# Performance work log

Measured on AMD Instinct MI355X. Metric: run time of the kernel, lower is better.

The kernel has to match this reference:

```python
import jax, jax.numpy as jnp
import numpy as np

B, T, I, H, NM = 128, 512, 2, 1024, 8
MS = H // NM  # module size = 128


def setup_inputs() -> dict:
    key = jax.random.key(0)
    ks = jax.random.split(key, 6)
    s = 1.0 / np.sqrt(H)
    return {
        "x": jax.random.normal(ks[0], (B, T + 1, I, 1), jnp.float32),
        "W_ih": jax.random.normal(ks[1], (H, I), jnp.float32) * s,
        "W_hh": jax.random.normal(ks[2], (H, H), jnp.float32) * s,
        "fc_w": jax.random.normal(ks[3], (I, H), jnp.float32) * s,
        "fc_b": jax.random.normal(ks[4], (I,), jnp.float32) * s,
        "enc_w": jax.random.normal(ks[5], (H, I), jnp.float32) * s,
    }


def reference(x, W_ih, W_hh, fc_w, fc_b, enc_w):
    # x: [B, T+1, I, 1] -> squeeze trailing dim
    xs = x[..., 0]                       # [B, T+1, I]
    h0 = xs[:, 0] @ enc_w.T              # start_encoder (no bias) -> [B, H]

    # Clockwork block structure: row-module i reads hidden cols >= i*MS.
    mod_idx = jnp.arange(H) // MS
    mask_hh = (mod_idx[None, :] >= mod_idx[:, None]).astype(W_hh.dtype)
    Whh_m = W_hh * mask_hh               # block upper-triangular recurrent weights
    periods = 2 ** jnp.arange(NM)        # module clock periods [1,2,4,...,128]

    def step(h, inp):
        x_t, t = inp                     # x_t: [B, I], t: scalar step index
        cand = jnp.tanh(x_t @ W_ih.T + h @ Whh_m.T)          # [B, H]
        active = jnp.repeat((t % periods) == 0, MS)          # [H] unit-level clock mask
        h_new = jnp.where(active[None, :], cand, h)          # inactive modules keep state
        return h_new, h_new @ fc_w.T + fc_b                  # fc output per step

    _, outs = jax.lax.scan(step, h0, (jnp.swapaxes(xs[:, 1:], 0, 1), jnp.arange(T)))
    return jnp.swapaxes(outs, 0, 1)      # [B, T, I]
```

## Files before the change

### kernel.cpp

```cpp
#include <hip/hip_runtime.h>
#include <hip/hip_fp16.h>
#include <math.h>

#define Bsz 128
#define Tsz 512
#define Hsz 1024
#define MS  128
#define NT  512


__global__ __launch_bounds__(256)
void retile_whh(const float* __restrict__ W, __half* __restrict__ WBr) {
    const int p = blockIdx.x + 1;
    const int t = threadIdx.x;
    int c = 0;
    while ((c+1)*(c+2)/2 <= p) ++c;
    const int r = p - c*(c+1)/2;
    __half* wb = WBr + (size_t)(p-1) * MS * MS;
    for (int o = t; o < MS*MS; o += 256) {
        const int k  = o >> 12;
        const int tt = (o >> 3) & 511;
        const int e  = o & 7;
        const int row = tt >> 2, jq = tt & 3;
        const int col = jq*32 + (((k + jq) & 3) << 3) + e;
        wb[o] = __float2half(W[(size_t)(r*MS+row)*Hsz + c*MS + col]);
    }
}

__device__ __forceinline__ float fast_tanh(float x) {
    const float e = __expf(2.0f * x);
    return 1.0f - 2.0f * __builtin_amdgcn_rcpf(e + 1.0f);
}

template <int CTRL>
__device__ __forceinline__ float dpp_get(float v) {
    union { float f; int i; } u, o;
    u.f = v;
    o.i = __builtin_amdgcn_update_dpp(0, u.i, CTRL, 0xf, 0xf, true);
    return o.f;
}

__device__ __forceinline__ void pk_fma(float2& acc, float2 a, float2 b) {
    asm("v_pk_fma_f32 %0, %1, %2, %0" : "+v"(acc) : "v"(a), "v"(b));
}

union H4 { short4 s4; __half2 h2[2]; };
union F4 { float4 v; float2 h[2]; };

__global__ __launch_bounds__(NT)
void cwrnn_kernel(const float* __restrict__ x,
                  const float* __restrict__ W_ih,
                  const float* __restrict__ fc_w,
                  const float* __restrict__ fc_b,
                  const float* __restrict__ enc_w,
                  const float* __restrict__ Whh,
                  const __half* __restrict__ WBr,
                  float* __restrict__ out)
{
    __shared__ __half  WL[3*MS*MS];
    __shared__ float   Sp2s[36][MS];
    __shared__ float   h_s[Hsz];
    __shared__ float   H0[2][MS];
    __shared__ float2  x_s[Tsz+1];
    __shared__ float2  wih_s[Hsz];
    __shared__ float2  fcw_s[Hsz];
    __shared__ float2  OpM0[2][8];
    __shared__ float2  OpHi[16];
    __shared__ float2  OpHiN[16];

    const int tid   = threadIdx.x;
    const int lane  = tid & 63;
    const int wave  = tid >> 6;
    const int b     = blockIdx.x;
    const int row00 = tid >> 2;
    const int jc    = tid & 3;

    const float2* xb = (const float2*)(x + (size_t)b*(Tsz+1)*2);
    float* outb = out + (size_t)b*Tsz*2;

    for (int i = tid; i < Tsz+1; i += NT) x_s[i] = xb[i];
    for (int i = tid; i < Hsz; i += NT) wih_s[i] = ((const float2*)W_ih)[i];
    for (int i = tid; i < Hsz; i += NT) fcw_s[i] = make_float2(fc_w[i], fc_w[Hsz+i]);
    {
        const int PSEL[3] = {2, 4, 5};
        for (int i = tid; i < 3*MS*MS/8; i += NT) {
            const int pi = i >> 11, rem = i & 2047;
            ((int4*)WL)[i] =
                ((const int4*)(WBr + (size_t)(PSEL[pi]-1)*MS*MS))[rem];
        }
    }
    if (tid < 16) { OpHi[tid] = make_float2(0.f,0.f); OpHiN[tid] = make_float2(0.f,0.f); }
    const float fb0 = fc_b[0], fb1 = fc_b[1];

    F4 w00[8];
    #pragma unroll
    for (int u = 0; u < 8; ++u) {
        const int uu = (u + 2*jc) & 7;
        w00[u].v = *(const float4*)(Whh + (size_t)row00*Hsz + jc*32 + uu*4);
    }
    short4 w01[8], w02[8];
    #pragma unroll
    for (int k = 0; k < 4; ++k) {
        *(int4*)(&w01[2*k]) = *(const int4*)(WBr + (size_t)0*MS*MS + k*4096 + tid*8);
        *(int4*)(&w02[2*k]) = *(const int4*)(WBr + (size_t)2*MS*MS + k*4096 + tid*8);
    }

    {
        const float2 x0 = xb[0];
        for (int i = tid; i < Hsz; i += NT) {
            const float2 ew = ((const float2*)enc_w)[i];
            const float v = x0.x*ew.x + x0.y*ew.y;
            h_s[i] = v;
            if (i < MS) H0[0][i] = v;
        }
    }
    __syncthreads();

    float R1=0.f,R2=0.f,R3=0.f,R4=0.f,R5=0.f,R6=0.f,R7=0.f;

    auto load_hq = [&](int c, F4* hq) {
        #pragma unroll
        for (int u = 0; u < 8; ++u) {
            const int uu = (u + 2*jc) & 7;
            hq[u].v = *(const float4*)(h_s + c*MS + jc*32 + uu*4);
        }
    };
    auto pair_acc16 = [&](const short4* w, const F4* hq) -> float {
        float2 a0 = {0.f,0.f}, a1 = {0.f,0.f};
        #pragma unroll
        for (int u = 0; u < 8; ++u) {
            H4 ww; ww.s4 = w[u];
            pk_fma(a0, __half22float2(ww.h2[0]), hq[u].h[0]);
            pk_fma(a1, __half22float2(ww.h2[1]), hq[u].h[1]);
        }
        return (a0.x + a0.y) + (a1.x + a1.y);
    };
    auto wl_read = [&](int pi, short4* w) {
        const __half* base = WL + (size_t)pi*MS*MS + tid*8;
        #pragma unroll
        for (int k = 0; k < 4; ++k)
            *(int4*)(&w[2*k]) = *(const int4*)(base + k*4096);
    };
    auto wg_load = [&](int p, short4* w) {
        const __half* base = WBr + (size_t)(p-1)*MS*MS + tid*8;
        #pragma unroll
        for (int k = 0; k < 4; ++k)
            *(int4*)(&w[2*k]) = *(const int4*)(base + k*4096);
    };

    auto do_cols = [&](int ashad) {
        F4 hq[8];
        short4 wA[8], wB[8];
        if (ashad >= 3) wg_load(6, wA);
        load_hq(1, hq);
        wl_read(0, wB);
        R1 = pair_acc16(w01, hq);
        { float aa = pair_acc16(wB, hq);
          aa += dpp_get<0xB1>(aa); aa += dpp_get<0x4E>(aa);
          if (jc == 0) Sp2s[2][row00] = aa; }
        if (ashad >= 2) {
            load_hq(2, hq);
            R2 = pair_acc16(w02, hq);
            wl_read(1, wB);
            { float aa = pair_acc16(wB, hq);
              aa += dpp_get<0xB1>(aa); aa += dpp_get<0x4E>(aa);
              if (jc == 0) Sp2s[4][row00] = aa; }
            wl_read(2, wB);
            { float aa = pair_acc16(wB, hq);
              aa += dpp_get<0xB1>(aa); aa += dpp_get<0x4E>(aa);
              if (jc == 0) Sp2s[5][row00] = aa; }
        }
        if (ashad >= 3) {
            load_hq(3, hq);
            int cc = 3, rr = 0;
            while (true) {
                int rn = rr + 1, cn = cc;
                if (rn > cn) { cn += 1; rn = 0; }
                const bool hn = (cn <= ashad);
                if (hn) wg_load(cn*(cn+1)/2 + rn, wB);
                float aa = pair_acc16(wA, hq);
                if (rr == 0) {
                    switch (cc) {
                        case 3: R3 = aa; break;
                        case 4: R4 = aa; break;
                        case 5: R5 = aa; break;
                        case 6: R6 = aa; break;
                        default: R7 = aa; break;
                    }
                } else {
                    aa += dpp_get<0xB1>(aa); aa += dpp_get<0x4E>(aa);
                    if (jc == 0) Sp2s[cc*(cc+1)/2 + rr][row00] = aa;
                }
                if (!hn) break;
                if (cn != cc) load_hq(cn, hq);
                cc = cn; rr = rn;
                #pragma unroll
                for (int u = 0; u < 8; ++u) wA[u] = wB[u];
            }
        }
    };

    do_cols(7);
    __syncthreads();

    for (int t = 0; t < Tsz; ++t) {
        const int A  = (t == 0) ? 7 : ((t & 1) ? 0 : min(__ffs(t)-1, 7));
        const int ap = (t & 1) ? ((t == 1) ? 7 : min(__ffs(t-1)-1, 7)) : 0;
        const float2 xt = x_s[t+1];

        if (ap >= 1) do_cols(ap);

        {
            const float* h0r = H0[t & 1];
            float2 a0 = {0.f,0.f}, a1 = {0.f,0.f};
            #pragma unroll
            for (int u = 0; u < 8; ++u) {
                const int uu = (u + 2*jc) & 7;
                F4 hv; hv.v = *(const float4*)(h0r + jc*32 + uu*4);
                pk_fma(a0, w00[u].h[0], hv.h[0]);
                pk_fma(a1, w00[u].h[1], hv.h[1]);
            }
            float a = (a0.x + a0.y) + (a1.x + a1.y);
            a += ((R1+R2)+(R3+R4)) + ((R5+R6)+R7);
            a += dpp_get<0xB1>(a); a += dpp_get<0x4E>(a);
            const float2 wih0 = wih_s[row00];
            const float hv0 = fast_tanh(a + xt.x*wih0.x + xt.y*wih0.y);
            if (jc == 0) H0[(t+1)&1][row00] = hv0;
            const float2 fw0 = fcw_s[row00];
            float o0 = (jc == 0) ? hv0*fw0.x : 0.f;
            float o1 = (jc == 0) ? hv0*fw0.y : 0.f;
            o0 += dpp_get<0x111>(o0); o1 += dpp_get<0x111>(o1);
            o0 += dpp_get<0x112>(o0); o1 += dpp_get<0x112>(o1);
            o0 += dpp_get<0x114>(o0); o1 += dpp_get<0x114>(o1);
            o0 += dpp_get<0x118>(o0); o1 += dpp_get<0x118>(o1);
            o0 += dpp_get<0x142>(o0); o1 += dpp_get<0x142>(o1);
            o0 += dpp_get<0x143>(o0); o1 += dpp_get<0x143>(o1);
            if (lane == 63) OpM0[t&1][wave] = make_float2(o0, o1);
        }

        if (A >= 1) {
            const int nrows = (A+1)*MS;
            {
                const int g = MS + tid;
                if (g < nrows) {
                    const int r = g >> 7, il = g & (MS-1);
                    float sc[8];
                    #pragma unroll
                    for (int c = 1; c < 8; ++c)
                        sc[c] = Sp2s[c*(c+1)/2 + ((c < r) ? c : r)][il];
                    const float2 wih2 = wih_s[g];
                    float pre = xt.x*wih2.x + xt.y*wih2.y;
                    #pragma unroll
                    for (int c = 1; c < 8; ++c) pre += (c >= r) ? sc[c] : 0.f;
                    const float hv = fast_tanh(pre);
                    h_s[g] = hv;
                    const float2 fw = fcw_s[g];
                    float o0 = hv*fw.x, o1 = hv*fw.y;
                    o0 += dpp_get<0x111>(o0); o1 += dpp_get<0x111>(o1);
                    o0 += dpp_get<0x112>(o0); o1 += dpp_get<0x112>(o1);
                    o0 += dpp_get<0x114>(o0); o1 += dpp_get<0x114>(o1);
                    o0 += dpp_get<0x118>(o0); o1 += dpp_get<0x118>(o1);
                    o0 += dpp_get<0x142>(o0); o1 += dpp_get<0x142>(o1);
                    o0 += dpp_get<0x143>(o0); o1 += dpp_get<0x143>(o1);
                    if (lane == 63) OpHiN[2 + wave] = make_float2(o0, o1);
                }
            }
            {
                const int g = 5*MS + tid;
                if (g < nrows) {
                    const int r = g >> 7, il = g & (MS-1);
                    float sc[8];
                    #pragma unroll
                    for (int c = 1; c < 8; ++c)
                        sc[c] = Sp2s[c*(c+1)/2 + ((c < r) ? c : r)][il];
                    const float2 wih2 = wih_s[g];
                    float pre = xt.x*wih2.x + xt.y*wih2.y;
                    #pragma unroll
                    for (int c = 1; c < 8; ++c) pre += (c >= r) ? sc[c] : 0.f;
                    const float hv = fast_tanh(pre);
                    h_s[g] = hv;
                    const float2 fw = fcw_s[g];
                    float o0 = hv*fw.x, o1 = hv*fw.y;
                    o0 += dpp_get<0x111>(o0); o1 += dpp_get<0x111>(o1);
                    o0 += dpp_get<0x112>(o0); o1 += dpp_get<0x112>(o1);
                    o0 += dpp_get<0x114>(o0); o1 += dpp_get<0x114>(o1);
                    o0 += dpp_get<0x118>(o0); o1 += dpp_get<0x118>(o1);
                    o0 += dpp_get<0x142>(o0); o1 += dpp_get<0x142>(o1);
                    o0 += dpp_get<0x143>(o0); o1 += dpp_get<0x143>(o1);
                    if (lane == 63) OpHiN[10 + wave] = make_float2(o0, o1);
                }
            }
        }

        if (t > 0 && tid == 0) {
            const int tp = t - 1;
            if (ap >= 1) {
                for (int k = 2; k <= 2*ap+1; ++k) OpHi[k] = OpHiN[k];
            }
            float o0 = fb0, o1 = fb1;
            #pragma unroll
            for (int w = 0; w < 8; ++w) { o0 += OpM0[tp&1][w].x; o1 += OpM0[tp&1][w].y; }
            #pragma unroll
            for (int k = 2; k < 16; ++k) { o0 += OpHi[k].x; o1 += OpHi[k].y; }
            *(float2*)(outb + 2*tp) = make_float2(o0, o1);
        }

        __syncthreads();
    }

    if (tid == 0) {
        float o0 = fb0, o1 = fb1;
        #pragma unroll
        for (int w = 0; w < 8; ++w) { o0 += OpM0[1][w].x; o1 += OpM0[1][w].y; }
        #pragma unroll
        for (int k = 2; k < 16; ++k) { o0 += OpHi[k].x; o1 += OpHi[k].y; }
        *(float2*)(outb + 2*(Tsz-1)) = make_float2(o0, o1);
    }
}

extern "C" void kernel_launch(void* const* d_in, const int* in_sizes, int n_in,
                              void* d_out, int out_size, void* d_ws, size_t ws_size,
                              hipStream_t stream) {
    const float* x     = (const float*)d_in[0];
    const float* W_ih  = (const float*)d_in[1];
    const float* W_hh  = (const float*)d_in[2];
    const float* fc_w  = (const float*)d_in[3];
    const float* fc_b  = (const float*)d_in[4];
    const float* enc_w = (const float*)d_in[5];
    float* outp = (float*)d_out;
    __half* WBr = (__half*)((char*)d_ws + 65536);

    retile_whh<<<35, 256, 0, stream>>>(W_hh, WBr);
    cwrnn_kernel<<<Bsz, NT, 0, stream>>>(x, W_ih, fc_w, fc_b, enc_w, W_hh, WBr, outp);
}
```

Baseline: 906.7 us.

## Double block threads to 1024 with 8 lanes per row and buffer outputs in LDS

Raises the per-batch workgroup from 512 to 1024 threads. Each hidden row is now split across 8 lanes instead of 4, so every thread holds half as many weights and h values, and the cross-lane reduction gains one extra DPP stage. The retile kernel's weight layout is changed to match the 8-lane split. The two per-thread row passes in the high-module update become a single pass, and the per-step output writes go into a shared buffer that is copied to global memory once at the end. The aim is to cut the per-thread serial FMA chain inside each latency-bound timestep. In exchange, each step's barriers now cover twice as many waves and the register budget per thread is tighter.

```diff
diff --git a/kernel.cpp b/kernel.cpp
--- a/kernel.cpp
+++ b/kernel.cpp
@@ -6,7 +6,7 @@
 #define Tsz 512
 #define Hsz 1024
 #define MS  128
-#define NT  512
+#define NT  1024
 
 
 __global__ __launch_bounds__(256)
@@ -18,11 +18,12 @@
     const int r = p - c*(c+1)/2;
     __half* wb = WBr + (size_t)(p-1) * MS * MS;
     for (int o = t; o < MS*MS; o += 256) {
-        const int k  = o >> 12;
-        const int tt = (o >> 3) & 511;
+        const int k  = o >> 13;
+        const int tt = (o >> 3) & 1023;
         const int e  = o & 7;
-        const int row = tt >> 2, jq = tt & 3;
-        const int col = jq*32 + (((k + jq) & 3) << 3) + e;
+        const int row = tt >> 3, jq = tt & 7;
+        const int chunk = ((2*k + (e >> 2)) + jq) & 3;
+        const int col = jq*16 + chunk*4 + (e & 3);
         wb[o] = __float2half(W[(size_t)(r*MS+row)*Hsz + c*MS + col]);
     }
 }
@@ -64,16 +65,16 @@
     __shared__ float2  x_s[Tsz+1];
     __shared__ float2  wih_s[Hsz];
     __shared__ float2  fcw_s[Hsz];
-    __shared__ float2  OpM0[2][8];
+    __shared__ float2  OpM0[2][16];
     __shared__ float2  OpHi[16];
     __shared__ float2  OpHiN[16];
+    __shared__ float   out_s[Tsz*2];
 
     const int tid   = threadIdx.x;
-    const int lane  = tid & 63;
     const int wave  = tid >> 6;
     const int b     = blockIdx.x;
-    const int row00 = tid >> 2;
-    const int jc    = tid & 3;
+    const int row00 = tid >> 3;
+    const int jc    = tid & 7;
 
     const float2* xb = (const float2*)(x + (size_t)b*(Tsz+1)*2);
     float* outb = out + (size_t)b*Tsz*2;
@@ -92,17 +93,17 @@
     if (tid < 16) { OpHi[tid] = make_float2(0.f,0.f); OpHiN[tid] = make_float2(0.f,0.f); }
     const float fb0 = fc_b[0], fb1 = fc_b[1];
 
-    F4 w00[8];
+    F4 w00[4];
     #pragma unroll
-    for (int u = 0; u < 8; ++u) {
-        const int uu = (u + 2*jc) & 7;
-        w00[u].v = *(const float4*)(Whh + (size_t)row00*Hsz + jc*32 + uu*4);
-    }
-    short4 w01[8], w02[8];
+    for (int u = 0; u < 4; ++u) {
+        const int uu = (u + jc) & 3;
+        w00[u].v = *(const float4*)(Whh + (size_t)row00*Hsz + jc*16 + uu*4);
+    }
+    short4 w01[4], w02[4];
     #pragma unroll
-    for (int k = 0; k < 4; ++k) {
-        *(int4*)(&w01[2*k]) = *(const int4*)(WBr + (size_t)0*MS*MS + k*4096 + tid*8);
-        *(int4*)(&w02[2*k]) = *(const int4*)(WBr + (size_t)2*MS*MS + k*4096 + tid*8);
+    for (int k = 0; k < 2; ++k) {
+        *(int4*)(&w01[2*k]) = *(const int4*)(WBr + (size_t)0*MS*MS + k*8192 + tid*8);
+        *(int4*)(&w02[2*k]) = *(const int4*)(WBr + (size_t)2*MS*MS + k*8192 + tid*8);
     }
 
     {
@@ -120,54 +121,57 @@
 
     auto load_hq = [&](int c, F4* hq) {
         #pragma unroll
-        for (int u = 0; u < 8; ++u) {
-            const int uu = (u + 2*jc) & 7;
-            hq[u].v = *(const float4*)(h_s + c*MS + jc*32 + uu*4);
+        for (int u = 0; u < 4; ++u) {
+            const int uu = (u + jc) & 3;
+            hq[u].v = *(const float4*)(h_s + c*MS + jc*16 + uu*4);
         }
     };
     auto pair_acc16 = [&](const short4* w, const F4* hq) -> float {
         float2 a0 = {0.f,0.f}, a1 = {0.f,0.f};
         #pragma unroll
-        for (int u = 0; u < 8; ++u) {
+        for (int u = 0; u < 4; ++u) {
             H4 ww; ww.s4 = w[u];
             pk_fma(a0, __half22float2(ww.h2[0]), hq[u].h[0]);
             pk_fma(a1, __half22float2(ww.h2[1]), hq[u].h[1]);
         }
         return (a0.x + a0.y) + (a1.x + a1.y);
     };
+    auto red8 = [&](float a) -> float {
+        a += dpp_get<0xB1>(a);
+        a += dpp_get<0x4E>(a);
+        a += dpp_get<0x141>(a);
+        return a;
+    };
     auto wl_read = [&](int pi, short4* w) {
         const __half* base = WL + (size_t)pi*MS*MS + tid*8;
         #pragma unroll
-        for (int k = 0; k < 4; ++k)
-            *(int4*)(&w[2*k]) = *(const int4*)(base + k*4096);
+        for (int k = 0; k < 2; ++k)
+            *(int4*)(&w[2*k]) = *(const int4*)(base + k*8192);
     };
     auto wg_load = [&](int p, short4* w) {
         const __half* base = WBr + (size_t)(p-1)*MS*MS + tid*8;
         #pragma unroll
-        for (int k = 0; k < 4; ++k)
-            *(int4*)(&w[2*k]) = *(const int4*)(base + k*4096);
+        for (int k = 0; k < 2; ++k)
+            *(int4*)(&w[2*k]) = *(const int4*)(base + k*8192);
     };
 
     auto do_cols = [&](int ashad) {
-        F4 hq[8];
-        short4 wA[8], wB[8];
+        F4 hq[4];
+        short4 wA[4], wB[4];
         if (ashad >= 3) wg_load(6, wA);
         load_hq(1, hq);
         wl_read(0, wB);
         R1 = pair_acc16(w01, hq);
-        { float aa = pair_acc16(wB, hq);
-          aa += dpp_get<0xB1>(aa); aa += dpp_get<0x4E>(aa);
+        { float aa = red8(pair_acc16(wB, hq));
           if (jc == 0) Sp2s[2][row00] = aa; }
         if (ashad >= 2) {
             load_hq(2, hq);
             R2 = pair_acc16(w02, hq);
             wl_read(1, wB);
-            { float aa = pair_acc16(wB, hq);
-              aa += dpp_get<0xB1>(aa); aa += dpp_get<0x4E>(aa);
+            { float aa = red8(pair_acc16(wB, hq));
               if (jc == 0) Sp2s[4][row00] = aa; }
             wl_read(2, wB);
-            { float aa = pair_acc16(wB, hq);
-              aa += dpp_get<0xB1>(aa); aa += dpp_get<0x4E>(aa);
+            { float aa = red8(pair_acc16(wB, hq));
               if (jc == 0) Sp2s[5][row00] = aa; }
         }
         if (ashad >= 3) {
@@ -188,14 +192,14 @@
                         default: R7 = aa; break;
                     }
                 } else {
-                    aa += dpp_get<0xB1>(aa); aa += dpp_get<0x4E>(aa);
+                    aa = red8(aa);
                     if (jc == 0) Sp2s[cc*(cc+1)/2 + rr][row00] = aa;
                 }
                 if (!hn) break;
                 if (cn != cc) load_hq(cn, hq);
                 cc = cn; rr = rn;
                 #pragma unroll
-                for (int u = 0; u < 8; ++u) wA[u] = wB[u];
+                for (int u = 0; u < 4; ++u) wA[u] = wB[u];
             }
         }
     };
@@ -214,15 +218,15 @@
             const float* h0r = H0[t & 1];
             float2 a0 = {0.f,0.f}, a1 = {0.f,0.f};
             #pragma unroll
-            for (int u = 0; u < 8; ++u) {
-                const int uu = (u + 2*jc) & 7;
-                F4 hv; hv.v = *(const float4*)(h0r + jc*32 + uu*4);
+            for (int u = 0; u < 4; ++u) {
+                const int uu = (u + jc) & 3;
+                F4 hv; hv.v = *(const float4*)(h0r + jc*16 + uu*4);
                 pk_fma(a0, w00[u].h[0], hv.h[0]);
                 pk_fma(a1, w00[u].h[1], hv.h[1]);
             }
             float a = (a0.x + a0.y) + (a1.x + a1.y);
             a += ((R1+R2)+(R3+R4)) + ((R5+R6)+R7);
-            a += dpp_get<0xB1>(a); a += dpp_get<0x4E>(a);
+            a = red8(a);
             const float2 wih0 = wih_s[row00];
             const float hv0 = fast_tanh(a + xt.x*wih0.x + xt.y*wih0.y);
             if (jc == 0) H0[(t+1)&1][row00] = hv0;
@@ -235,87 +239,64 @@
             o0 += dpp_get<0x118>(o0); o1 += dpp_get<0x118>(o1);
             o0 += dpp_get<0x142>(o0); o1 += dpp_get<0x142>(o1);
             o0 += dpp_get<0x143>(o0); o1 += dpp_get<0x143>(o1);
-            if (lane == 63) OpM0[t&1][wave] = make_float2(o0, o1);
+            if ((tid & 63) == 63) OpM0[t&1][wave] = make_float2(o0, o1);
         }
 
         if (A >= 1) {
             const int nrows = (A+1)*MS;
-            {
-                const int g = MS + tid;
-                if (g < nrows) {
-                    const int r = g >> 7, il = g & (MS-1);
-                    float sc[8];
-                    #pragma unroll
-                    for (int c = 1; c < 8; ++c)
-                        sc[c] = Sp2s[c*(c+1)/2 + ((c < r) ? c : r)][il];
-                    const float2 wih2 = wih_s[g];
-                    float pre = xt.x*wih2.x + xt.y*wih2.y;
-                    #pragma unroll
-                    for (int c = 1; c < 8; ++c) pre += (c >= r) ? sc[c] : 0.f;
-                    const float hv = fast_tanh(pre);
-                    h_s[g] = hv;
-                    const float2 fw = fcw_s[g];
-                    float o0 = hv*fw.x, o1 = hv*fw.y;
-                    o0 += dpp_get<0x111>(o0); o1 += dpp_get<0x111>(o1);
-                    o0 += dpp_get<0x112>(o0); o1 += dpp_get<0x112>(o1);
-                    o0 += dpp_get<0x114>(o0); o1 += dpp_get<0x114>(o1);
-                    o0 += dpp_get<0x118>(o0); o1 += dpp_get<0x118>(o1);
-                    o0 += dpp_get<0x142>(o0); o1 += dpp_get<0x142>(o1);
-                    o0 += dpp_get<0x143>(o0); o1 += dpp_get<0x143>(o1);
-                    if (lane == 63) OpHiN[2 + wave] = make_float2(o0, o1);
-                }
+            const int g = MS + tid;
+            if (g < nrows) {
+                const int r = g >> 7, il = g & (MS-1);
+                float sc[8];
+                #pragma unroll
+                for (int c = 1; c < 8; ++c)
+                    sc[c] = Sp2s[c*(c+1)/2 + ((c < r) ? c : r)][il];
+                const float2 wih2 = wih_s[g];
+                float pre = xt.x*wih2.x + xt.y*wih2.y;
+                #pragma unroll
+                for (int c = 1; c < 8; ++c) pre += (c >= r) ? sc[c] : 0.f;
+                const float hv = fast_tanh(pre);
+                h_s[g] = hv;
+                const float2 fw = fcw_s[g];
+                float o0 = hv*fw.x, o1 = hv*fw.y;
+                o0 += dpp_get<0x111>(o0); o1 += dpp_get<0x111>(o1);
+                o0 += dpp_get<0x112>(o0); o1 += dpp_get<0x112>(o1);
+                o0 += dpp_get<0x114>(o0); o1 += dpp_get<0x114>(o1);
+                o0 += dpp_get<0x118>(o0); o1 += dpp_get<0x118>(o1);
+                o0 += dpp_get<0x142>(o0); o1 += dpp_get<0x142>(o1);
+                o0 += dpp_get<0x143>(o0); o1 += dpp_get<0x143>(o1);
+                if ((tid & 63) == 63) OpHiN[2 + wave] = make_float2(o0, o1);
             }
-            {
-                const int g = 5*MS + tid;
-                if (g < nrows) {
-                    const int r = g >> 7, il = g & (MS-1);
-                    float sc[8];
-                    #pragma unroll
-                    for (int c = 1; c < 8; ++c)
-                        sc[c] = Sp2s[c*(c+1)/2 + ((c < r) ? c : r)][il];
-                    const float2 wih2 = wih_s[g];
-                    float pre = xt.x*wih2.x + xt.y*wih2.y;
-                    #pragma unroll
-                    for (int c = 1; c < 8; ++c) pre += (c >= r) ? sc[c] : 0.f;
-                    const float hv = fast_tanh(pre);
-                    h_s[g] = hv;
-                    const float2 fw = fcw_s[g];
-                    float o0 = hv*fw.x, o1 = hv*fw.y;
-                    o0 += dpp_get<0x111>(o0); o1 += dpp_get<0x111>(o1);
-                    o0 += dpp_get<0x112>(o0); o1 += dpp_get<0x112>(o1);
-                    o0 += dpp_get<0x114>(o0); o1 += dpp_get<0x114>(o1);
-                    o0 += dpp_get<0x118>(o0); o1 += dpp_get<0x118>(o1);
-                    o0 += dpp_get<0x142>(o0); o1 += dpp_get<0x142>(o1);
-                    o0 += dpp_get<0x143>(o0); o1 += dpp_get<0x143>(o1);
-                    if (lane == 63) OpHiN[10 + wave] = make_float2(o0, o1);
-                }
-            }
-        }
-
-        if (t > 0 && tid == 0) {
+        }
+
+        if (t > 0 && tid == 960) {
             const int tp = t - 1;
             if (ap >= 1) {
                 for (int k = 2; k <= 2*ap+1; ++k) OpHi[k] = OpHiN[k];
             }
             float o0 = fb0, o1 = fb1;
             #pragma unroll
-            for (int w = 0; w < 8; ++w) { o0 += OpM0[tp&1][w].x; o1 += OpM0[tp&1][w].y; }
+            for (int w = 0; w < 16; ++w) { o0 += OpM0[tp&1][w].x; o1 += OpM0[tp&1][w].y; }
             #pragma unroll
             for (int k = 2; k < 16; ++k) { o0 += OpHi[k].x; o1 += OpHi[k].y; }
-            *(float2*)(outb + 2*tp) = make_float2(o0, o1);
+            out_s[2*tp]   = o0;
+            out_s[2*tp+1] = o1;
         }
 
         __syncthreads();
     }
 
-    if (tid == 0) {
+    if (tid == 960) {
         float o0 = fb0, o1 = fb1;
         #pragma unroll
-        for (int w = 0; w < 8; ++w) { o0 += OpM0[1][w].x; o1 += OpM0[1][w].y; }
+        for (int w = 0; w < 16; ++w) { o0 += OpM0[1][w].x; o1 += OpM0[1][w].y; }
         #pragma unroll
         for (int k = 2; k < 16; ++k) { o0 += OpHi[k].x; o1 += OpHi[k].y; }
-        *(float2*)(outb + 2*(Tsz-1)) = make_float2(o0, o1);
-    }
+        out_s[2*(Tsz-1)]   = o0;
+        out_s[2*(Tsz-1)+1] = o1;
+    }
+    __syncthreads();
+    for (int i = tid; i < Tsz*2; i += NT) outb[i] = out_s[i];
 }
 
 extern "C" void kernel_launch(void* const* d_in, const int* in_sizes, int n_in,
```

Measured after the change: 1.125 ms. +24.1%, slower.
